# Optimization experiments

Hardware: AMD Instinct MI355X
Metric: run time of the kernel (lower is better)

Reference implementation:

```python
import jax, jax.numpy as jnp
import numpy as np

B, S, D, H = 4, 2048, 1024, 16
DK = D // H

def setup_inputs() -> dict:
    key = jax.random.key(0)
    ks = jax.random.split(key, 5)
    x = jax.random.normal(ks[0], (B, S, D), dtype=jnp.float32)
    scale = 1.0 / np.sqrt(D)
    Wq = jax.random.normal(ks[1], (D, D), dtype=jnp.float32) * scale
    Wk = jax.random.normal(ks[2], (D, D), dtype=jnp.float32) * scale
    Wv = jax.random.normal(ks[3], (D, D), dtype=jnp.float32) * scale
    Wo = jax.random.normal(ks[4], (D, D), dtype=jnp.float32) * scale
    return {"x": x, "Wq": Wq, "Wk": Wk, "Wv": Wv, "Wo": Wo}

def reference(x, Wq, Wk, Wv, Wo):
    # F.linear: y = x @ W.T  (weights stored torch-style [out, in])
    q = jnp.einsum('bsd,ed->bse', x, Wq).reshape(B, S, H, DK).transpose(0, 2, 1, 3)
    k = jnp.einsum('bsd,ed->bse', x, Wk).reshape(B, S, H, DK).transpose(0, 2, 1, 3)
    v = jnp.einsum('bsd,ed->bse', x, Wv).reshape(B, S, H, DK).transpose(0, 2, 1, 3)
    scores = jnp.einsum('bhqd,bhkd->bhqk', q, k) / jnp.sqrt(jnp.float32(DK))
    attn = jax.nn.softmax(scores, axis=-1)  # dropout p=0.0 -> identity
    out = jnp.einsum('bhqk,bhkd->bhqd', attn, v)
    out = out.transpose(0, 2, 1, 3).reshape(B, S, D)
    return jnp.einsum('bsd,ed->bse', out, Wo)
```

## Files before the change

kernel.cpp:

```cpp
#include <hip/hip_runtime.h>
#include <hip/hip_bf16.h>

#define B_ 4
#define S_ 2048
#define D_ 1024
#define H_ 16
#define DK_ 64

typedef __attribute__((ext_vector_type(8))) short short8;
typedef __attribute__((ext_vector_type(4))) float floatx4;
typedef __attribute__((ext_vector_type(16))) float floatx16;
typedef __attribute__((ext_vector_type(4))) unsigned int uint4v;

#define QSCL 0.1803368801111204f

static __device__ __forceinline__ unsigned short f2bf(float f) {
    unsigned int u = __float_as_uint(f);
    u += 0x7fffu + ((u >> 16) & 1u);
    return (unsigned short)(u >> 16);
}

static __device__ __forceinline__ unsigned int pack2bf_perm(float a, float b) {
    unsigned int u0 = __float_as_uint(a) + 0x8000u;
    unsigned int u1 = __float_as_uint(b) + 0x8000u;
    return __builtin_amdgcn_perm(u1, u0, 0x07060302u);
}

static __device__ __forceinline__ unsigned int pack2bf(float a, float b) {
    return (unsigned int)f2bf(a) | ((unsigned int)f2bf(b) << 16);
}

#define PLSWAP(a, b) asm volatile("v_permlane32_swap_b32 %0, %1" : "+v"(a), "+v"(b))

struct CastAll {
    const float* x;
    const float* w[4];
    unsigned short* xd;
    unsigned short* wd[4];
};

__global__ void cast_all_kernel(CastAll a) {
    int i = blockIdx.x * blockDim.x + threadIdx.x;
    const float* s;
    unsigned short* d;
    int j;
    if (i < 2097152) {
        s = a.x; d = a.xd; j = i;
    } else {
        int k = i - 2097152;
        int w = k >> 18;
        j = k & 262143;
        s = a.w[w]; d = a.wd[w];
    }
    float4 v = ((const float4*)s)[j];
    ushort4 o;
    o.x = f2bf(v.x); o.y = f2bf(v.y); o.z = f2bf(v.z); o.w = f2bf(v.w);
    ((ushort4*)d)[j] = o;
}

template <typename OutT, bool VT2>
__global__ __launch_bounds__(256) void gemm_bt(
    const unsigned short* __restrict__ A,
    const unsigned short* __restrict__ W0,
    const unsigned short* __restrict__ W1,
    const unsigned short* __restrict__ W2,
    OutT* __restrict__ C0, OutT* __restrict__ C1, OutT* __restrict__ C2,
    int M, int N, int K)
{
    __shared__ __align__(16) unsigned short At[128 * 64];
    __shared__ __align__(16) unsigned short Bt[128 * 64];

    const unsigned short* W = (blockIdx.z == 0) ? W0 : ((blockIdx.z == 1) ? W1 : W2);
    OutT* C = (blockIdx.z == 0) ? C0 : ((blockIdx.z == 1) ? C1 : C2);

    const int m0 = blockIdx.x * 128;
    const int n0 = blockIdx.y * 128;
    const int wv = threadIdx.x >> 6;
    const int ln = threadIdx.x & 63;
    const int l31 = ln & 31;
    const int half = ln >> 5;
    const int wm = (wv >> 1) * 64;
    const int wn = (wv & 1) * 64;

    floatx16 acc[2][2];
#pragma unroll
    for (int mt = 0; mt < 2; mt++)
#pragma unroll
        for (int nt = 0; nt < 2; nt++)
#pragma unroll
            for (int e = 0; e < 16; e++) acc[mt][nt][e] = 0.f;

    const int lr = ln >> 3;
    const int lc = (((ln & 7) ^ lr) * 8);
    const int sw = (l31 & 7);

    for (int k0 = 0; k0 < K; k0 += 64) {
        __syncthreads();
#pragma unroll
        for (int c = 0; c < 4; c++) {
            int rowA = wv * 32 + c * 8;
            const unsigned short* gA = A + (size_t)(m0 + rowA + lr) * K + k0 + lc;
            __builtin_amdgcn_global_load_lds(
                (const __attribute__((address_space(1))) void*)gA,
                (__attribute__((address_space(3))) void*)&At[rowA * 64], 16, 0, 0);
            const unsigned short* gB = W + (size_t)(n0 + rowA + lr) * K + k0 + lc;
            __builtin_amdgcn_global_load_lds(
                (const __attribute__((address_space(1))) void*)gB,
                (__attribute__((address_space(3))) void*)&Bt[rowA * 64], 16, 0, 0);
        }
        __syncthreads();

#pragma unroll
        for (int ks = 0; ks < 4; ks++) {
            const int slot = ((ks * 2 + half) ^ sw) * 8;
            short8 af[2], bf[2];
#pragma unroll
            for (int mt = 0; mt < 2; mt++)
                af[mt] = *(const short8*)&At[(wm + mt * 32 + l31) * 64 + slot];
#pragma unroll
            for (int nt = 0; nt < 2; nt++)
                bf[nt] = *(const short8*)&Bt[(wn + nt * 32 + l31) * 64 + slot];
#pragma unroll
            for (int mt = 0; mt < 2; mt++)
#pragma unroll
                for (int nt = 0; nt < 2; nt++)
                    acc[mt][nt] = __builtin_amdgcn_mfma_f32_32x32x16_bf16(af[mt], bf[nt], acc[mt][nt], 0, 0, 0);
        }
    }

    const float esc = (VT2 && blockIdx.z == 0) ? QSCL : 1.0f;

    if constexpr (VT2) {
        if (blockIdx.z == 2) {
            unsigned short* Vt = (unsigned short*)C;
#pragma unroll
            for (int mt = 0; mt < 2; mt++)
#pragma unroll
                for (int nt = 0; nt < 2; nt++)
#pragma unroll
                    for (int rg = 0; rg < 4; rg++) {
                        int col = n0 + wn + nt * 32 + l31;
                        int row0 = m0 + wm + mt * 32 + 4 * half + 8 * rg;
                        int bb = row0 >> 11, ss = row0 & 2047;
                        size_t addr = ((size_t)(bb * 1024 + col)) * 2048 + ss;
                        uint2 pk;
                        pk.x = pack2bf(acc[mt][nt][4 * rg + 0], acc[mt][nt][4 * rg + 1]);
                        pk.y = pack2bf(acc[mt][nt][4 * rg + 2], acc[mt][nt][4 * rg + 3]);
                        *(uint2*)(Vt + addr) = pk;
                    }
            return;
        }
    }

#pragma unroll
    for (int mt = 0; mt < 2; mt++)
#pragma unroll
        for (int nt = 0; nt < 2; nt++)
#pragma unroll
            for (int rg = 0; rg < 4; rg++)
#pragma unroll
                for (int r = 0; r < 4; r++) {
                    int row = m0 + wm + mt * 32 + 4 * half + 8 * rg + r;
                    int col = n0 + wn + nt * 32 + l31;
                    float v = acc[mt][nt][4 * rg + r] * esc;
                    if constexpr (sizeof(OutT) == 2)
                        C[(size_t)row * N + col] = (OutT)f2bf(v);
                    else
                        C[(size_t)row * N + col] = v;
                }
}

__global__ __launch_bounds__(512, 4) void flash_attn(
    const unsigned short* __restrict__ Q,
    const unsigned short* __restrict__ K,
    const unsigned short* __restrict__ Vt,
    unsigned short* __restrict__ O)
{
    __shared__ __align__(16) unsigned short Kt[2][64 * 72];
    __shared__ __align__(16) unsigned short VT[2][64 * 72];

    const int pair = blockIdx.x;
    const int h = pair & 15;
    const int b = pair >> 4;
    const int qt = blockIdx.y;
    const int tid = threadIdx.x;
    const int wv = tid >> 6;
    const int ln = tid & 63;
    const int l31 = ln & 31;
    const int half = ln >> 5;

    const size_t base = ((size_t)b * S_) * D_ + (size_t)h * DK_;
    const size_t vtbase = ((size_t)(b * 1024 + h * 64)) * (size_t)S_;

    const int qrow = qt * 256 + wv * 32 + l31;
    short8 qf[4];
    {
        const unsigned short* qp = Q + base + (size_t)qrow * D_ + half * 8;
#pragma unroll
        for (int ks = 0; ks < 4; ks++) qf[ks] = *(const short8*)(qp + ks * 16);
    }

    floatx16 Oacc[2];
#pragma unroll
    for (int mt = 0; mt < 2; mt++)
#pragma unroll
        for (int e = 0; e < 16; e++) Oacc[mt][e] = 0.f;
    float l_i = 0.f;

    const int srow = tid >> 3;
    const int scol = (tid & 7) * 8;
    const unsigned short* kp = K + base + (size_t)srow * D_ + scol;
    const unsigned short* vp = Vt + vtbase + (size_t)srow * S_ + scol;
    const int swo = srow * 72 + scol;

    short8 kr = *(const short8*)kp;
    short8 vr = *(const short8*)vp;
    kp += (size_t)64 * D_;
    vp += 64;

    for (int kt = 0; kt < S_ / 64; kt++) {
        const int cb = kt & 1;
        unsigned short* Kc = &Kt[cb][0];
        unsigned short* Vc = &VT[cb][0];
        *(short8*)&Kc[swo] = kr;
        *(short8*)&Vc[swo] = vr;
        __syncthreads();

        if (kt < S_ / 64 - 1) {
            kr = *(const short8*)kp;
            vr = *(const short8*)vp;
            kp += (size_t)64 * D_;
            vp += 64;
        }

        uint2 run[2][4];

#pragma unroll
        for (int mt = 0; mt < 2; mt++) {
            floatx16 sac;
#pragma unroll
            for (int e = 0; e < 16; e++) sac[e] = 0.f;
            __builtin_amdgcn_s_setprio(1);
#pragma unroll
            for (int ks = 0; ks < 4; ks++) {
                short8 kf = *(const short8*)&Kc[(mt * 32 + l31) * 72 + ks * 16 + half * 8];
                sac = __builtin_amdgcn_mfma_f32_32x32x16_bf16(kf, qf[ks], sac, 0, 0, 0);
            }
            __builtin_amdgcn_s_setprio(0);
#pragma unroll
            for (int g = 0; g < 4; g++) {
                float p0 = __builtin_amdgcn_exp2f(sac[4 * g + 0]);
                float p1 = __builtin_amdgcn_exp2f(sac[4 * g + 1]);
                float p2 = __builtin_amdgcn_exp2f(sac[4 * g + 2]);
                float p3 = __builtin_amdgcn_exp2f(sac[4 * g + 3]);
                l_i += (p0 + p1) + (p2 + p3);
                run[mt][g].x = pack2bf_perm(p0, p1);
                run[mt][g].y = pack2bf_perm(p2, p3);
            }
        }

#pragma unroll
        for (int mt = 0; mt < 2; mt++)
#pragma unroll
            for (int t = 0; t < 2; t++) {
                PLSWAP(run[mt][2 * t].x, run[mt][2 * t + 1].x);
                PLSWAP(run[mt][2 * t].y, run[mt][2 * t + 1].y);
            }

#pragma unroll
        for (int mt2 = 0; mt2 < 2; mt2++)
#pragma unroll
            for (int t = 0; t < 2; t++) {
                int ks = mt2 * 2 + t;
                uint4v u = {run[mt2][2 * t].x, run[mt2][2 * t].y,
                            run[mt2][2 * t + 1].x, run[mt2][2 * t + 1].y};
                short8 pf = __builtin_bit_cast(short8, u);
                __builtin_amdgcn_s_setprio(1);
#pragma unroll
                for (int mt = 0; mt < 2; mt++) {
                    short8 vf = *(const short8*)&Vc[(mt * 32 + l31) * 72 + ks * 16 + half * 8];
                    Oacc[mt] = __builtin_amdgcn_mfma_f32_32x32x16_bf16(vf, pf, Oacc[mt], 0, 0, 0);
                }
                __builtin_amdgcn_s_setprio(0);
            }
    }

    {
        float ls = l_i + __shfl_xor(l_i, 32);
        float inv = 1.0f / ls;
        const size_t orow = base + (size_t)qrow * D_;
#pragma unroll
        for (int mt = 0; mt < 2; mt++)
#pragma unroll
            for (int g = 0; g < 4; g++) {
                uint2 pk;
                pk.x = pack2bf(Oacc[mt][4 * g + 0] * inv, Oacc[mt][4 * g + 1] * inv);
                pk.y = pack2bf(Oacc[mt][4 * g + 2] * inv, Oacc[mt][4 * g + 3] * inv);
                *(uint2*)(O + orow + mt * 32 + 8 * g + 4 * half) = pk;
            }
    }
}

extern "C" void kernel_launch(void* const* d_in, const int* in_sizes, int n_in,
                              void* d_out, int out_size, void* d_ws, size_t ws_size,
                              hipStream_t stream) {
    const float* x  = (const float*)d_in[0];
    const float* Wq = (const float*)d_in[1];
    const float* Wk = (const float*)d_in[2];
    const float* Wv = (const float*)d_in[3];
    const float* Wo = (const float*)d_in[4];
    float* out = (float*)d_out;

    char* ws = (char*)d_ws;
    const size_t MB = 1024 * 1024;
    unsigned short* xb  = (unsigned short*)(ws);
    unsigned short* wqb = (unsigned short*)(ws + 16 * MB);
    unsigned short* wkb = (unsigned short*)(ws + 18 * MB);
    unsigned short* wvb = (unsigned short*)(ws + 20 * MB);
    unsigned short* wob = (unsigned short*)(ws + 22 * MB);
    unsigned short* Qb  = (unsigned short*)(ws + 24 * MB);
    unsigned short* Kb  = (unsigned short*)(ws + 40 * MB);
    unsigned short* Vtb = (unsigned short*)(ws + 56 * MB);
    unsigned short* Ob  = (unsigned short*)(ws);

    CastAll ca;
    ca.x = x; ca.xd = xb;
    ca.w[0] = Wq; ca.w[1] = Wk; ca.w[2] = Wv; ca.w[3] = Wo;
    ca.wd[0] = wqb; ca.wd[1] = wkb; ca.wd[2] = wvb; ca.wd[3] = wob;
    cast_all_kernel<<<12288, 256, 0, stream>>>(ca);

    dim3 gq((B_ * S_) / 128, D_ / 128, 3);
    gemm_bt<unsigned short, true><<<gq, 256, 0, stream>>>(
        xb, wqb, wkb, wvb, Qb, Kb, Vtb, B_ * S_, D_, D_);

    dim3 gf(64, S_ / 256, 1);
    flash_attn<<<gf, 512, 0, stream>>>(Qb, Kb, Vtb, Ob);

    dim3 go((B_ * S_) / 128, D_ / 128, 1);
    gemm_bt<float, false><<<go, 256, 0, stream>>>(
        Ob, wob, wob, wob, out, out, out, B_ * S_, D_, D_);
}
```

Before: 269.8 us.

## Enlarge GEMM tiles to 256x256 with double-buffered LDS prefetch

The projection GEMMs move from 128x128 tiles with 4 waves to 256x256 tiles with 8 waves, each wave computing a 128x64 sub-tile. The LDS is double-buffered so the next K-slice is loaded asynchronously while MFMAs run on the current one, and s_setprio raises wave priority around the MFMA bursts. This aims to raise arithmetic intensity and hide global-load latency. The cost is far fewer blocks: the QKV GEMM drops to 384 blocks and the output GEMM to 128, which may underfill the GPU's 256 CUs, and 128KB of LDS per block limits occupancy.

```diff
diff --git a/kernel.cpp b/kernel.cpp
--- a/kernel.cpp
+++ b/kernel.cpp
@@ -59,7 +59,7 @@
 }
 
 template <typename OutT, bool VT2>
-__global__ __launch_bounds__(256) void gemm_bt(
+__global__ __launch_bounds__(512, 1) void gemm_bt(
     const unsigned short* __restrict__ A,
     const unsigned short* __restrict__ W0,
     const unsigned short* __restrict__ W1,
@@ -67,66 +67,93 @@
     OutT* __restrict__ C0, OutT* __restrict__ C1, OutT* __restrict__ C2,
     int M, int N, int K)
 {
-    __shared__ __align__(16) unsigned short At[128 * 64];
-    __shared__ __align__(16) unsigned short Bt[128 * 64];
+    __shared__ __align__(16) unsigned short At[2][256 * 64];
+    __shared__ __align__(16) unsigned short Bt[2][256 * 64];
 
     const unsigned short* W = (blockIdx.z == 0) ? W0 : ((blockIdx.z == 1) ? W1 : W2);
     OutT* C = (blockIdx.z == 0) ? C0 : ((blockIdx.z == 1) ? C1 : C2);
 
-    const int m0 = blockIdx.x * 128;
-    const int n0 = blockIdx.y * 128;
-    const int wv = threadIdx.x >> 6;
-    const int ln = threadIdx.x & 63;
+    const int m0 = blockIdx.x * 256;
+    const int n0 = blockIdx.y * 256;
+    const int tid = threadIdx.x;
+    const int wv = tid >> 6;
+    const int ln = tid & 63;
     const int l31 = ln & 31;
     const int half = ln >> 5;
-    const int wm = (wv >> 1) * 64;
-    const int wn = (wv & 1) * 64;
-
-    floatx16 acc[2][2];
-#pragma unroll
-    for (int mt = 0; mt < 2; mt++)
+    const int wm = (wv >> 2) * 128;
+    const int wn = (wv & 3) * 64;
+
+    floatx16 acc[4][2];
+#pragma unroll
+    for (int am = 0; am < 4; am++)
 #pragma unroll
         for (int nt = 0; nt < 2; nt++)
 #pragma unroll
-            for (int e = 0; e < 16; e++) acc[mt][nt][e] = 0.f;
+            for (int e = 0; e < 16; e++) acc[am][nt][e] = 0.f;
 
     const int lr = ln >> 3;
     const int lc = (((ln & 7) ^ lr) * 8);
     const int sw = (l31 & 7);
 
-    for (int k0 = 0; k0 < K; k0 += 64) {
-        __syncthreads();
-#pragma unroll
-        for (int c = 0; c < 4; c++) {
-            int rowA = wv * 32 + c * 8;
-            const unsigned short* gA = A + (size_t)(m0 + rowA + lr) * K + k0 + lc;
-            __builtin_amdgcn_global_load_lds(
-                (const __attribute__((address_space(1))) void*)gA,
-                (__attribute__((address_space(3))) void*)&At[rowA * 64], 16, 0, 0);
-            const unsigned short* gB = W + (size_t)(n0 + rowA + lr) * K + k0 + lc;
-            __builtin_amdgcn_global_load_lds(
-                (const __attribute__((address_space(1))) void*)gB,
-                (__attribute__((address_space(3))) void*)&Bt[rowA * 64], 16, 0, 0);
-        }
-        __syncthreads();
-
+#define STAGE(dbuf, k0)                                                                     \
+    {                                                                                       \
+        _Pragma("unroll")                                                                   \
+        for (int u = 0; u < 4; u++) {                                                       \
+            const unsigned short* src = (u < 2) ? A : W;                                    \
+            unsigned short* dst = (u < 2) ? &At[dbuf][0] : &Bt[dbuf][0];                    \
+            const int base0 = (u < 2) ? m0 : n0;                                            \
+            const int hf = u & 1;                                                           \
+            _Pragma("unroll")                                                               \
+            for (int j = 0; j < 2; j++) {                                                   \
+                const int rowb = hf * 128 + j * 64 + wv * 8;                                \
+                const unsigned short* g = src + (size_t)(base0 + rowb + lr) * K + (k0) + lc;\
+                __builtin_amdgcn_global_load_lds(                                           \
+                    (const __attribute__((address_space(1))) void*)g,                       \
+                    (__attribute__((address_space(3))) void*)&dst[rowb * 64], 16, 0, 0);    \
+            }                                                                               \
+        }                                                                                   \
+    }
+
+    STAGE(0, 0);
+    __syncthreads();
+
+    const int NT = K / 64;
+    for (int t = 0; t < NT; t++) {
+        const int d = t & 1;
+        if (t + 1 < NT) STAGE(d ^ 1, (t + 1) * 64);
+
+        short8 bfr[2][4];
 #pragma unroll
         for (int ks = 0; ks < 4; ks++) {
             const int slot = ((ks * 2 + half) ^ sw) * 8;
-            short8 af[2], bf[2];
-#pragma unroll
-            for (int mt = 0; mt < 2; mt++)
-                af[mt] = *(const short8*)&At[(wm + mt * 32 + l31) * 64 + slot];
 #pragma unroll
             for (int nt = 0; nt < 2; nt++)
-                bf[nt] = *(const short8*)&Bt[(wn + nt * 32 + l31) * 64 + slot];
-#pragma unroll
-            for (int mt = 0; mt < 2; mt++)
-#pragma unroll
-                for (int nt = 0; nt < 2; nt++)
-                    acc[mt][nt] = __builtin_amdgcn_mfma_f32_32x32x16_bf16(af[mt], bf[nt], acc[mt][nt], 0, 0, 0);
-        }
-    }
+                bfr[nt][ks] = *(const short8*)&Bt[d][(wn + nt * 32 + l31) * 64 + slot];
+        }
+#pragma unroll
+        for (int qm = 0; qm < 2; qm++) {
+            short8 af[2][4];
+#pragma unroll
+            for (int ks = 0; ks < 4; ks++) {
+                const int slot = ((ks * 2 + half) ^ sw) * 8;
+#pragma unroll
+                for (int mt = 0; mt < 2; mt++)
+                    af[mt][ks] = *(const short8*)&At[d][(wm + (qm * 2 + mt) * 32 + l31) * 64 + slot];
+            }
+            __builtin_amdgcn_s_setprio(1);
+#pragma unroll
+            for (int ks = 0; ks < 4; ks++)
+#pragma unroll
+                for (int mt = 0; mt < 2; mt++)
+#pragma unroll
+                    for (int nt = 0; nt < 2; nt++)
+                        acc[qm * 2 + mt][nt] = __builtin_amdgcn_mfma_f32_32x32x16_bf16(
+                            af[mt][ks], bfr[nt][ks], acc[qm * 2 + mt][nt], 0, 0, 0);
+            __builtin_amdgcn_s_setprio(0);
+        }
+        __syncthreads();
+    }
+#undef STAGE
 
     const float esc = (VT2 && blockIdx.z == 0) ? QSCL : 1.0f;
 
@@ -134,18 +161,18 @@
         if (blockIdx.z == 2) {
             unsigned short* Vt = (unsigned short*)C;
 #pragma unroll
-            for (int mt = 0; mt < 2; mt++)
+            for (int am = 0; am < 4; am++)
 #pragma unroll
                 for (int nt = 0; nt < 2; nt++)
 #pragma unroll
                     for (int rg = 0; rg < 4; rg++) {
                         int col = n0 + wn + nt * 32 + l31;
-                        int row0 = m0 + wm + mt * 32 + 4 * half + 8 * rg;
+                        int row0 = m0 + wm + am * 32 + 4 * half + 8 * rg;
                         int bb = row0 >> 11, ss = row0 & 2047;
                         size_t addr = ((size_t)(bb * 1024 + col)) * 2048 + ss;
                         uint2 pk;
-                        pk.x = pack2bf(acc[mt][nt][4 * rg + 0], acc[mt][nt][4 * rg + 1]);
-                        pk.y = pack2bf(acc[mt][nt][4 * rg + 2], acc[mt][nt][4 * rg + 3]);
+                        pk.x = pack2bf(acc[am][nt][4 * rg + 0], acc[am][nt][4 * rg + 1]);
+                        pk.y = pack2bf(acc[am][nt][4 * rg + 2], acc[am][nt][4 * rg + 3]);
                         *(uint2*)(Vt + addr) = pk;
                     }
             return;
@@ -153,16 +180,16 @@
     }
 
 #pragma unroll
-    for (int mt = 0; mt < 2; mt++)
+    for (int am = 0; am < 4; am++)
 #pragma unroll
         for (int nt = 0; nt < 2; nt++)
 #pragma unroll
             for (int rg = 0; rg < 4; rg++)
 #pragma unroll
                 for (int r = 0; r < 4; r++) {
-                    int row = m0 + wm + mt * 32 + 4 * half + 8 * rg + r;
+                    int row = m0 + wm + am * 32 + 4 * half + 8 * rg + r;
                     int col = n0 + wn + nt * 32 + l31;
-                    float v = acc[mt][nt][4 * rg + r] * esc;
+                    float v = acc[am][nt][4 * rg + r] * esc;
                     if constexpr (sizeof(OutT) == 2)
                         C[(size_t)row * N + col] = (OutT)f2bf(v);
                     else
@@ -329,14 +356,14 @@
     ca.wd[0] = wqb; ca.wd[1] = wkb; ca.wd[2] = wvb; ca.wd[3] = wob;
     cast_all_kernel<<<12288, 256, 0, stream>>>(ca);
 
-    dim3 gq((B_ * S_) / 128, D_ / 128, 3);
-    gemm_bt<unsigned short, true><<<gq, 256, 0, stream>>>(
+    dim3 gq((B_ * S_) / 256, D_ / 256, 3);
+    gemm_bt<unsigned short, true><<<gq, 512, 0, stream>>>(
         xb, wqb, wkb, wvb, Qb, Kb, Vtb, B_ * S_, D_, D_);
 
     dim3 gf(64, S_ / 256, 1);
     flash_attn<<<gf, 512, 0, stream>>>(Qb, Kb, Vtb, Ob);
 
-    dim3 go((B_ * S_) / 128, D_ / 128, 1);
-    gemm_bt<float, false><<<go, 256, 0, stream>>>(
+    dim3 go((B_ * S_) / 256, D_ / 256, 1);
+    gemm_bt<float, false><<<go, 512, 0, stream>>>(
         Ob, wob, wob, wob, out, out, out, B_ * S_, D_, D_);
 }
```

Result: slower. 290.9 us (+7.8%).

## Triple-buffer GEMM LDS tiles with async prefetch and 256x128 block tiles

Applied to the files above, without the earlier changes.

Rewrites the projection GEMM main loop to keep three LDS stages, issuing global-to-LDS loads two k-tiles ahead and syncing with explicit vmcnt waits and raw barriers instead of two __syncthreads per step. Blocks grow to 512 threads covering 256x128 output tiles. All LDS fragments for a k-tile are loaded before the MFMA burst, which runs at raised priority. The goal is to hide global load latency behind MFMA work, at the cost of much more LDS per block (~144KB), one block per CU, and half as many blocks in the grid.

```diff
diff --git a/kernel.cpp b/kernel.cpp
--- a/kernel.cpp
+++ b/kernel.cpp
@@ -31,6 +31,8 @@
 }
 
 #define PLSWAP(a, b) asm volatile("v_permlane32_swap_b32 %0, %1" : "+v"(a), "+v"(b))
+
+#define SW_VMCNT(N) asm volatile("s_waitcnt vmcnt(" #N ")" ::: "memory")
 
 struct CastAll {
     const float* x;
@@ -59,7 +61,7 @@
 }
 
 template <typename OutT, bool VT2>
-__global__ __launch_bounds__(256) void gemm_bt(
+__global__ __launch_bounds__(512, 1) void gemm_bt(
     const unsigned short* __restrict__ A,
     const unsigned short* __restrict__ W0,
     const unsigned short* __restrict__ W1,
@@ -67,16 +69,17 @@
     OutT* __restrict__ C0, OutT* __restrict__ C1, OutT* __restrict__ C2,
     int M, int N, int K)
 {
-    __shared__ __align__(16) unsigned short At[128 * 64];
-    __shared__ __align__(16) unsigned short Bt[128 * 64];
+    __shared__ __align__(16) unsigned short At[3][256 * 64];
+    __shared__ __align__(16) unsigned short Bt[3][128 * 64];
 
     const unsigned short* W = (blockIdx.z == 0) ? W0 : ((blockIdx.z == 1) ? W1 : W2);
     OutT* C = (blockIdx.z == 0) ? C0 : ((blockIdx.z == 1) ? C1 : C2);
 
-    const int m0 = blockIdx.x * 128;
+    const int m0 = blockIdx.x * 256;
     const int n0 = blockIdx.y * 128;
-    const int wv = threadIdx.x >> 6;
-    const int ln = threadIdx.x & 63;
+    const int tid = threadIdx.x;
+    const int wv = tid >> 6;
+    const int ln = tid & 63;
     const int l31 = ln & 31;
     const int half = ln >> 5;
     const int wm = (wv >> 1) * 64;
@@ -94,39 +97,70 @@
     const int lc = (((ln & 7) ^ lr) * 8);
     const int sw = (l31 & 7);
 
-    for (int k0 = 0; k0 < K; k0 += 64) {
-        __syncthreads();
-#pragma unroll
-        for (int c = 0; c < 4; c++) {
-            int rowA = wv * 32 + c * 8;
-            const unsigned short* gA = A + (size_t)(m0 + rowA + lr) * K + k0 + lc;
-            __builtin_amdgcn_global_load_lds(
-                (const __attribute__((address_space(1))) void*)gA,
-                (__attribute__((address_space(3))) void*)&At[rowA * 64], 16, 0, 0);
-            const unsigned short* gB = W + (size_t)(n0 + rowA + lr) * K + k0 + lc;
-            __builtin_amdgcn_global_load_lds(
-                (const __attribute__((address_space(1))) void*)gB,
-                (__attribute__((address_space(3))) void*)&Bt[rowA * 64], 16, 0, 0);
-        }
-        __syncthreads();
-
+#define STAGE(db, k0)                                                                       \
+    {                                                                                       \
+        _Pragma("unroll")                                                                   \
+        for (int i = 0; i < 4; i++) {                                                       \
+            const int rowb = wv * 32 + i * 8;                                               \
+            const unsigned short* g = A + (size_t)(m0 + rowb + lr) * K + (k0) + lc;         \
+            __builtin_amdgcn_global_load_lds(                                               \
+                (const __attribute__((address_space(1))) void*)g,                           \
+                (__attribute__((address_space(3))) void*)&At[db][rowb * 64], 16, 0, 0);     \
+        }                                                                                   \
+        _Pragma("unroll")                                                                   \
+        for (int i = 0; i < 2; i++) {                                                       \
+            const int rowb = wv * 16 + i * 8;                                               \
+            const unsigned short* g = W + (size_t)(n0 + rowb + lr) * K + (k0) + lc;         \
+            __builtin_amdgcn_global_load_lds(                                               \
+                (const __attribute__((address_space(1))) void*)g,                           \
+                (__attribute__((address_space(3))) void*)&Bt[db][rowb * 64], 16, 0, 0);     \
+        }                                                                                   \
+    }
+
+    const int NT = K / 64;
+    STAGE(0, 0);
+    STAGE(1, 64);
+    SW_VMCNT(6);
+    __builtin_amdgcn_s_barrier();
+
+    int cur = 0;
+    for (int t = 0; t < NT; t++) {
+        if (t + 2 < NT) {
+            int stg = cur + 2; if (stg >= 3) stg -= 3;
+            STAGE(stg, (t + 2) * 64);
+        }
+
+        short8 af[2][4], bfr[2][4];
 #pragma unroll
         for (int ks = 0; ks < 4; ks++) {
             const int slot = ((ks * 2 + half) ^ sw) * 8;
-            short8 af[2], bf[2];
+#pragma unroll
+            for (int nt = 0; nt < 2; nt++)
+                bfr[nt][ks] = *(const short8*)&Bt[cur][(wn + nt * 32 + l31) * 64 + slot];
 #pragma unroll
             for (int mt = 0; mt < 2; mt++)
-                af[mt] = *(const short8*)&At[(wm + mt * 32 + l31) * 64 + slot];
-#pragma unroll
-            for (int nt = 0; nt < 2; nt++)
-                bf[nt] = *(const short8*)&Bt[(wn + nt * 32 + l31) * 64 + slot];
+                af[mt][ks] = *(const short8*)&At[cur][(wm + mt * 32 + l31) * 64 + slot];
+        }
+
+        __builtin_amdgcn_s_setprio(1);
+#pragma unroll
+        for (int ks = 0; ks < 4; ks++)
 #pragma unroll
             for (int mt = 0; mt < 2; mt++)
 #pragma unroll
                 for (int nt = 0; nt < 2; nt++)
-                    acc[mt][nt] = __builtin_amdgcn_mfma_f32_32x32x16_bf16(af[mt], bf[nt], acc[mt][nt], 0, 0, 0);
-        }
-    }
+                    acc[mt][nt] = __builtin_amdgcn_mfma_f32_32x32x16_bf16(
+                        af[mt][ks], bfr[nt][ks], acc[mt][nt], 0, 0, 0);
+        __builtin_amdgcn_s_setprio(0);
+
+        if (t + 1 < NT) {
+            if (t + 2 < NT) { SW_VMCNT(6); }
+            else            { SW_VMCNT(0); }
+            __builtin_amdgcn_s_barrier();
+        }
+        cur = (cur == 2) ? 0 : cur + 1;
+    }
+#undef STAGE
 
     const float esc = (VT2 && blockIdx.z == 0) ? QSCL : 1.0f;
 
@@ -329,14 +363,14 @@
     ca.wd[0] = wqb; ca.wd[1] = wkb; ca.wd[2] = wvb; ca.wd[3] = wob;
     cast_all_kernel<<<12288, 256, 0, stream>>>(ca);
 
-    dim3 gq((B_ * S_) / 128, D_ / 128, 3);
-    gemm_bt<unsigned short, true><<<gq, 256, 0, stream>>>(
+    dim3 gq((B_ * S_) / 256, D_ / 128, 3);
+    gemm_bt<unsigned short, true><<<gq, 512, 0, stream>>>(
         xb, wqb, wkb, wvb, Qb, Kb, Vtb, B_ * S_, D_, D_);
 
     dim3 gf(64, S_ / 256, 1);
     flash_attn<<<gf, 512, 0, stream>>>(Qb, Kb, Vtb, Ob);
 
-    dim3 go((B_ * S_) / 128, D_ / 128, 1);
-    gemm_bt<float, false><<<go, 256, 0, stream>>>(
+    dim3 go((B_ * S_) / 256, D_ / 128, 1);
+    gemm_bt<float, false><<<go, 512, 0, stream>>>(
         Ob, wob, wob, wob, out, out, out, B_ * S_, D_, D_);
 }
```

Result: slower. 282.4 us (+4.7%).

## Split flash attention KV sequence across two warp groups per block

Applied to the files above, without the earlier changes.

Doubles the flash attention block to 1024 threads. Two groups of 8 waves each process half of the key/value sequence (1024 keys each) for the same 256 query rows, and each group keeps its own double-buffered K/V tiles in shared memory. At the end, group 1 writes its partial output accumulators and row sums to LDS and group 0 adds them before normalizing. This halves the serial KV loop length per wave and adds wave-level parallelism, at the cost of a cross-group reduction, more LDS, and block-wide syncs shared by both groups. The combine drops the running max and simply sums partials, which is only correct if the softmax uses a fixed, non-max-subtracted exponent (the hidden loop appears to track only l_i).

```diff
diff --git a/kernel.cpp b/kernel.cpp
--- a/kernel.cpp
+++ b/kernel.cpp
@@ -170,14 +170,13 @@
                 }
 }
 
-__global__ __launch_bounds__(512, 4) void flash_attn(
+__global__ __launch_bounds__(1024, 2) void flash_attn(
     const unsigned short* __restrict__ Q,
     const unsigned short* __restrict__ K,
     const unsigned short* __restrict__ Vt,
     unsigned short* __restrict__ O)
 {
-    __shared__ __align__(16) unsigned short Kt[2][64 * 72];
-    __shared__ __align__(16) unsigned short VT[2][64 * 72];
+    __shared__ __align__(16) unsigned short KVs[2][2][2][64 * 72];
 
     const int pair = blockIdx.x;
     const int h = pair & 15;
@@ -185,6 +184,8 @@
     const int qt = blockIdx.y;
     const int tid = threadIdx.x;
     const int wv = tid >> 6;
+    const int wg = wv >> 3;
+    const int wl = wv & 7;
     const int ln = tid & 63;
     const int l31 = ln & 31;
     const int half = ln >> 5;
@@ -192,7 +193,7 @@
     const size_t base = ((size_t)b * S_) * D_ + (size_t)h * DK_;
     const size_t vtbase = ((size_t)(b * 1024 + h * 64)) * (size_t)S_;
 
-    const int qrow = qt * 256 + wv * 32 + l31;
+    const int qrow = qt * 256 + wl * 32 + l31;
     short8 qf[4];
     {
         const unsigned short* qp = Q + base + (size_t)qrow * D_ + half * 8;
@@ -207,10 +208,11 @@
         for (int e = 0; e < 16; e++) Oacc[mt][e] = 0.f;
     float l_i = 0.f;
 
-    const int srow = tid >> 3;
-    const int scol = (tid & 7) * 8;
-    const unsigned short* kp = K + base + (size_t)srow * D_ + scol;
-    const unsigned short* vp = Vt + vtbase + (size_t)srow * S_ + scol;
+    const int gtid = tid & 511;
+    const int srow = gtid >> 3;
+    const int scol = (gtid & 7) * 8;
+    const unsigned short* kp = K + base + (size_t)(wg * 1024 + srow) * D_ + scol;
+    const unsigned short* vp = Vt + vtbase + (size_t)srow * S_ + wg * 1024 + scol;
     const int swo = srow * 72 + scol;
 
     short8 kr = *(const short8*)kp;
@@ -218,15 +220,15 @@
     kp += (size_t)64 * D_;
     vp += 64;
 
-    for (int kt = 0; kt < S_ / 64; kt++) {
+    for (int kt = 0; kt < 16; kt++) {
         const int cb = kt & 1;
-        unsigned short* Kc = &Kt[cb][0];
-        unsigned short* Vc = &VT[cb][0];
+        unsigned short* Kc = &KVs[wg][cb][0][0];
+        unsigned short* Vc = &KVs[wg][cb][1][0];
         *(short8*)&Kc[swo] = kr;
         *(short8*)&Vc[swo] = vr;
         __syncthreads();
 
-        if (kt < S_ / 64 - 1) {
+        if (kt < 15) {
             kr = *(const short8*)kp;
             vr = *(const short8*)vp;
             kp += (size_t)64 * D_;
@@ -285,17 +287,33 @@
             }
     }
 
-    {
+    __syncthreads();
+    float* ex = (float*)&KVs[0][0][0][0];
+    const int idx = (wl * 64 + ln) * 33;
+    if (wg == 1) {
+        float ls1 = l_i + __shfl_xor(l_i, 32);
+#pragma unroll
+        for (int mt = 0; mt < 2; mt++)
+#pragma unroll
+            for (int e = 0; e < 16; e++) ex[idx + mt * 16 + e] = Oacc[mt][e];
+        ex[idx + 32] = ls1;
+    }
+    __syncthreads();
+    if (wg == 0) {
         float ls = l_i + __shfl_xor(l_i, 32);
-        float inv = 1.0f / ls;
+        float inv = 1.0f / (ls + ex[idx + 32]);
         const size_t orow = base + (size_t)qrow * D_;
 #pragma unroll
         for (int mt = 0; mt < 2; mt++)
 #pragma unroll
             for (int g = 0; g < 4; g++) {
+                float o0 = (Oacc[mt][4 * g + 0] + ex[idx + mt * 16 + 4 * g + 0]) * inv;
+                float o1 = (Oacc[mt][4 * g + 1] + ex[idx + mt * 16 + 4 * g + 1]) * inv;
+                float o2 = (Oacc[mt][4 * g + 2] + ex[idx + mt * 16 + 4 * g + 2]) * inv;
+                float o3 = (Oacc[mt][4 * g + 3] + ex[idx + mt * 16 + 4 * g + 3]) * inv;
                 uint2 pk;
-                pk.x = pack2bf(Oacc[mt][4 * g + 0] * inv, Oacc[mt][4 * g + 1] * inv);
-                pk.y = pack2bf(Oacc[mt][4 * g + 2] * inv, Oacc[mt][4 * g + 3] * inv);
+                pk.x = pack2bf(o0, o1);
+                pk.y = pack2bf(o2, o3);
                 *(uint2*)(O + orow + mt * 32 + 8 * g + 4 * half) = pk;
             }
     }
@@ -334,7 +352,7 @@
         xb, wqb, wkb, wvb, Qb, Kb, Vtb, B_ * S_, D_, D_);
 
     dim3 gf(64, S_ / 256, 1);
-    flash_attn<<<gf, 512, 0, stream>>>(Qb, Kb, Vtb, Ob);
+    flash_attn<<<gf, 1024, 0, stream>>>(Qb, Kb, Vtb, Ob);
 
     dim3 go((B_ * S_) / 128, D_ / 128, 1);
     gemm_bt<float, false><<<go, 256, 0, stream>>>(
```

Result: no change. 272.0 us (+0.8%).
